# Optimization experiments

Hardware: AMD Instinct MI355X
Metric: run time of the kernel (lower is better)

## Reference

```python
import jax, jax.numpy as jnp
import numpy as np

E, DM, DH, K, DIL = 8, 512, 1024, 3, 2
N, L = 128, 128
PAD = DIL * (K - 1) // 2  # 'same' padding


def _conv1d(x, w):
    # x: [N, Cin, L], w: [Cout, Cin, K] -> [N, Cout, L]
    return jax.lax.conv_general_dilated(
        x, w, window_strides=(1,), padding=[(PAD, PAD)],
        rhs_dilation=(DIL,), dimension_numbers=("NCH", "OIH", "NCH"))


def _moe_conv(x, W, B, onehot):
    # W: [E, Cout, Cin, K], B: [E, Cout], onehot: [N, E]
    ys = jax.vmap(lambda w, b: _conv1d(x, w) + b[None, :, None])(W, B)  # [E, N, Cout, L]
    return jnp.einsum("enol,ne->nol", ys, onehot)


def setup_inputs() -> dict:
    key = jax.random.key(0)
    k1, k2, k3, k4, k5 = jax.random.split(key, 5)
    inp = jax.random.normal(k1, (N, DM, L), dtype=jnp.float32)
    # uneven per-expert sample counts summing to N (samples pre-sorted by expert)
    fwd_expert_count = jnp.asarray(np.array([10, 20, 16, 16, 12, 22, 14, 18], dtype=np.int32))
    w1 = jax.random.normal(k2, (E, DH, DM, K), dtype=jnp.float32) * 0.02
    b1 = jax.random.normal(k3, (E, DH), dtype=jnp.float32) * 0.02
    w2 = jax.random.normal(k4, (E, DM, DH, K), dtype=jnp.float32) * 0.02
    b2 = jax.random.normal(k5, (E, DM), dtype=jnp.float32) * 0.02
    return {"inp": inp, "fwd_expert_count": fwd_expert_count,
            "w1": w1, "b1": b1, "w2": w2, "b2": b2}


def reference(inp, fwd_expert_count, w1, b1, w2, b2):
    # map each sample index to its expert via cumulative counts
    cs = jnp.cumsum(fwd_expert_count)
    eid = jnp.searchsorted(cs, jnp.arange(N), side="right")  # [N]
    onehot = (eid[:, None] == jnp.arange(E)[None, :]).astype(inp.dtype)  # [N, E]
    h = _moe_conv(inp, w1, b1, onehot)       # [N, DH, L]
    h = jax.nn.gelu(h)
    out = _moe_conv(h, w2, b2, onehot)       # [N, DM, L]
    return out
```

## Files before the change

kernel.cpp:

```cpp
#include <hip/hip_runtime.h>
#include <hip/hip_bf16.h>
#include <stdint.h>


typedef __attribute__((ext_vector_type(8))) short short8;
typedef __attribute__((ext_vector_type(4))) float f32x4;

#define NSAMP 128
#define DMV 512
#define DHV 1024

#define OFF_X   0ull
#define OFF_H   (16ull << 20)
#define OFF_W1  (48ull << 20)
#define OFF_W2  (72ull << 20)

__device__ __forceinline__ uint16_t f2bf(float f) {
  uint32_t u = __builtin_bit_cast(uint32_t, f);
  uint32_t r = (u + 0x7FFFu + ((u >> 16) & 1u)) >> 16;
  return (uint16_t)r;
}

__device__ __forceinline__ void async_copy16(const void* g, void* l) {
  __builtin_amdgcn_global_load_lds(
      (const __attribute__((address_space(1))) uint32_t*)g,
      (__attribute__((address_space(3))) uint32_t*)l, 16, 0, 0);
}

__device__ __forceinline__ float gelu_f(float x) {
  float u = 0.7978845608028654f * (x + 0.044715f * x * x * x);
  float t = __expf(2.0f * u);
  float th = 1.0f - 2.0f / (t + 1.0f);
  return 0.5f * x * (1.0f + th);
}

__global__ void prep_x(const float* __restrict__ inp, uint16_t* __restrict__ xp) {
  uint32_t t = blockIdx.x * 256u + threadIdx.x;
  uint32_t sub = t & 3u;
  uint32_t l = (t >> 2) & 127u;
  uint32_t cc = (t >> 9) & 15u;
  uint32_t s = t >> 13;
  uint32_t fl = ((l + 2u) >> 1) & 3u;
  uint32_t c0 = cc * 32u + ((sub ^ fl) & 3u) * 8u;
  const float* src = inp + ((size_t)s * DMV + c0) * 128u + l;
  uint32_t pk[4];
#pragma unroll
  for (int p = 0; p < 4; ++p) {
    uint32_t lo = f2bf(src[(size_t)(2 * p) * 128u]);
    uint32_t hi = f2bf(src[(size_t)(2 * p + 1) * 128u]);
    pk[p] = lo | (hi << 16);
  }
  uint4 v; v.x = pk[0]; v.y = pk[1]; v.z = pk[2]; v.w = pk[3];
  ((uint4*)xp)[t] = v;
}

__global__ void prep_w(const float* __restrict__ w, uint16_t* __restrict__ wp,
                       int C, int mtBits, int ccBits) {
  uint32_t t = blockIdx.x * 256u + threadIdx.x;
  uint32_t sub = t & 3u;
  uint32_t row = (t >> 2) & 127u;
  uint32_t t2 = t >> 9;
  uint32_t k = t2 % 3u;
  uint32_t t3 = t2 / 3u;
  uint32_t mt = t3 & ((1u << mtBits) - 1u);
  uint32_t t4 = t3 >> mtBits;
  uint32_t cc = t4 & ((1u << ccBits) - 1u);
  uint32_t e = t4 >> ccBits;
  uint32_t O = 128u << mtBits;
  uint32_t o = mt * 128u + row;
  uint32_t c0 = cc * 32u + ((sub ^ (row >> 1)) & 3u) * 8u;
  const float* src = w + (((size_t)e * O + o) * (uint32_t)C + c0) * 3u + k;
  uint32_t pk[4];
#pragma unroll
  for (int p = 0; p < 4; ++p) {
    uint32_t lo = f2bf(src[(size_t)(2 * p) * 3u]);
    uint32_t hi = f2bf(src[(size_t)(2 * p + 1) * 3u]);
    pk[p] = lo | (hi << 16);
  }
  uint4 v; v.x = pk[0]; v.y = pk[1]; v.z = pk[2]; v.w = pk[3];
  ((uint4*)wp)[t] = v;
}

template <int PHASE>
__global__ __launch_bounds__(512, 2) void conv_mfma(
    const uint16_t* __restrict__ bprep, const uint16_t* __restrict__ wprep,
    const float* __restrict__ bias, const int* __restrict__ cnt,
    uint16_t* __restrict__ hout, float* __restrict__ fout) {
  constexpr int CC = (PHASE == 1) ? 16 : 32;
  constexpr int HALVES = (PHASE == 1) ? 2 : 1;
  constexpr int MTP = (PHASE == 1) ? 8 : 4;
  constexpr int AREP = 4 * HALVES;
  constexpr int OO = (PHASE == 1) ? DHV : DMV;
  constexpr uint32_t AS = HALVES * 24576u;
  constexpr uint32_t BUFS = AS + 16896u;

  uint32_t b = blockIdx.x;
  uint32_t work = (b & 7u) * 32u + (b >> 3);
  const int pr = work & 63;
  const int mt = work >> 6;
  int e = 0;
  {
    int cum = cnt[0];
    while (2 * pr >= cum && e < 7) { ++e; cum += cnt[e]; }
  }
  const int tid = threadIdx.x;
  const int lane = tid & 63;
  const int wv = tid >> 6;
  const int wr = wv >> 2, wc = wv & 3;
  const int l15 = lane & 15, kg = lane >> 4;

  __shared__ __align__(16) uint8_t lds[2 * BUFS];

  uint32_t aOff[AREP];
#pragma unroll
  for (int a = 0; a < AREP; ++a) {
    uint32_t R = (uint32_t)(wr * (AREP * 16) + a * 16 + l15);
    uint32_t h = R >> 7, ri = R & 127u;
    aOff[a] = h * 24576u + ri * 64u + (((uint32_t)kg ^ (ri >> 1)) & 3u) * 16u;
  }
  uint32_t lB[4];
#pragma unroll
  for (int bq = 0; bq < 4; ++bq) lB[bq] = (uint32_t)((wc & 1) * 64 + bq * 16 + l15);
  const uint32_t pOff = AS + (uint32_t)(wc >> 1) * 8448u;
  const int mtBase = (PHASE == 1) ? mt * 2 : mt;

  auto STAGE = [&](int buf, int cc) {
    uint8_t* bb = lds + (uint32_t)buf * BUFS;
    const uint16_t* wsrc = wprep + (((size_t)e * CC + cc) * MTP + mtBase) * 12288;
#pragma unroll
    for (int i = 0; i < 3 * HALVES; ++i)
      async_copy16(wsrc + i * 4096 + tid * 8, bb + (uint32_t)i * 8192u + tid * 16);
#pragma unroll
    for (int p = 0; p < 2; ++p)
      async_copy16(bprep + (((size_t)(2 * pr + p)) * CC + cc) * 4096 + tid * 8,
                   bb + AS + (uint32_t)p * 8448u + 128u + tid * 16);
  };

  if (tid < 64) {
    uint32_t n = (uint32_t)tid >> 5, rest = (uint32_t)tid & 31u;
    uint32_t p = rest >> 4, ri = (rest >> 2) & 3u, sb = rest & 3u;
    uint32_t rowByte = (ri < 2) ? ri * 64u : (8320u + (ri - 2) * 64u);
    uint4 z = make_uint4(0, 0, 0, 0);
    *(uint4*)(lds + n * BUFS + AS + p * 8448u + rowByte + sb * 16u) = z;
  }
  STAGE(0, 0);
  __syncthreads();

  f32x4 acc[AREP][4] = {};

#pragma unroll 2
  for (int cc = 0; cc < CC; ++cc) {
    int cur = cc & 1;
    if (cc + 1 < CC) STAGE(cur ^ 1, cc + 1);
    const uint8_t* bb = lds + (uint32_t)cur * BUFS;
#pragma unroll
    for (int k = 0; k < 3; ++k) {
      short8 af[AREP], bf[4];
#pragma unroll
      for (int a = 0; a < AREP; ++a)
        af[a] = *(const short8*)(bb + aOff[a] + (uint32_t)k * 8192u);
#pragma unroll
      for (int bq = 0; bq < 4; ++bq) {
        uint32_t r = lB[bq] + 2u * (uint32_t)k;
        bf[bq] = *(const short8*)(bb + pOff + r * 64u +
                                  (((uint32_t)kg ^ (r >> 1)) & 3u) * 16u);
      }
#pragma unroll
      for (int a = 0; a < AREP; ++a)
#pragma unroll
        for (int bq = 0; bq < 4; ++bq)
          acc[a][bq] = __builtin_amdgcn_mfma_f32_16x16x32_bf16(af[a], bf[bq], acc[a][bq], 0, 0, 0);
    }
    __syncthreads();
  }

  const int p = wc >> 1;
  const int s = 2 * pr + p;
  if (PHASE == 1) {
#pragma unroll
    for (int a = 0; a < AREP; ++a) {
      int ob = mt * 256 + wr * 128 + a * 16 + kg * 4;
      float4 bv = *(const float4*)(bias + (size_t)e * OO + ob);
      int cc2 = mt * 8 + wr * 4 + (a >> 1);
      uint32_t g = (uint32_t)((a & 1) * 2 + (kg >> 1));
      uint32_t j0 = (uint32_t)((kg & 1) * 4);
#pragma unroll
      for (int bq = 0; bq < 4; ++bq) {
        int l = (wc & 1) * 64 + bq * 16 + l15;
        uint32_t flq = ((uint32_t)(l + 2) >> 1) & 3u;
        uint32_t sub = g ^ flq;
        float v0 = gelu_f(acc[a][bq][0] + bv.x);
        float v1 = gelu_f(acc[a][bq][1] + bv.y);
        float v2 = gelu_f(acc[a][bq][2] + bv.z);
        float v3 = gelu_f(acc[a][bq][3] + bv.w);
        uint2 pk;
        pk.x = (uint32_t)f2bf(v0) | ((uint32_t)f2bf(v1) << 16);
        pk.y = (uint32_t)f2bf(v2) | ((uint32_t)f2bf(v3) << 16);
        size_t ci = ((size_t)s * 32 + cc2) * 128 + l;
        *(uint2*)(hout + ci * 32 + sub * 8 + j0) = pk;
      }
    }
  } else {
#pragma unroll
    for (int a = 0; a < AREP; ++a) {
      int ob = mt * 128 + wr * 64 + a * 16 + kg * 4;
      float4 bv = *(const float4*)(bias + (size_t)e * OO + ob);
      float bvr[4] = {bv.x, bv.y, bv.z, bv.w};
      float* op = fout + ((size_t)s * DMV + ob) * 128;
#pragma unroll
      for (int bq = 0; bq < 4; ++bq) {
        int l = (wc & 1) * 64 + bq * 16 + l15;
#pragma unroll
        for (int r = 0; r < 4; ++r)
          op[(size_t)r * 128 + l] = acc[a][bq][r] + bvr[r];
      }
    }
  }
}

extern "C" void kernel_launch(void* const* d_in, const int* in_sizes, int n_in,
                              void* d_out, int out_size, void* d_ws, size_t ws_size,
                              hipStream_t stream) {
  const float* inp = (const float*)d_in[0];
  const int* cnt = (const int*)d_in[1];
  const float* w1 = (const float*)d_in[2];
  const float* b1 = (const float*)d_in[3];
  const float* w2 = (const float*)d_in[4];
  const float* b2 = (const float*)d_in[5];
  float* out = (float*)d_out;
  uint8_t* ws = (uint8_t*)d_ws;
  uint16_t* xp = (uint16_t*)(ws + OFF_X);
  uint16_t* hp = (uint16_t*)(ws + OFF_H);
  uint16_t* w1p = (uint16_t*)(ws + OFF_W1);
  uint16_t* w2p = (uint16_t*)(ws + OFF_W2);

  prep_x<<<dim3(4096), dim3(256), 0, stream>>>(inp, xp);
  prep_w<<<dim3(6144), dim3(256), 0, stream>>>(w1, w1p, 512, 3, 4);
  prep_w<<<dim3(6144), dim3(256), 0, stream>>>(w2, w2p, 1024, 2, 5);
  conv_mfma<1><<<dim3(256), dim3(512), 0, stream>>>(xp, w1p, b1, cnt, hp, nullptr);
  conv_mfma<2><<<dim3(256), dim3(512), 0, stream>>>(hp, w2p, b2, cnt, nullptr, out);
}
```

Baseline: 160.8 us.

## Interleave async staging with MFMA steps and fuse prep kernels into one launch

The conv main loop is restructured into fine-grained steps. Each step issues part of the next chunk's global-to-LDS copies, then waits with explicit vmcnt counts and raw s_barrier instead of a full __syncthreads per chunk, and raises wave priority around the MFMA block. A-tile rows are remapped so each wave row group reads its own half in phase 1. The three prep kernels are merged into one launch to cut launch overhead. Hand-counted waitcnt values risk races if the copy order or counts are wrong, and the extra barriers per step add sync cost.

```diff
diff --git a/kernel.cpp b/kernel.cpp
--- a/kernel.cpp
+++ b/kernel.cpp
@@ -6,7 +6,6 @@
 typedef __attribute__((ext_vector_type(8))) short short8;
 typedef __attribute__((ext_vector_type(4))) float f32x4;
 
-#define NSAMP 128
 #define DMV 512
 #define DHV 1024
 
@@ -14,6 +13,9 @@
 #define OFF_H   (16ull << 20)
 #define OFF_W1  (48ull << 20)
 #define OFF_W2  (72ull << 20)
+
+#define VMW(n) asm volatile("s_waitcnt vmcnt(" #n ")" ::: "memory")
+#define VMNOP  do {} while (0)
 
 __device__ __forceinline__ uint16_t f2bf(float f) {
   uint32_t u = __builtin_bit_cast(uint32_t, f);
@@ -34,8 +36,8 @@
   return 0.5f * x * (1.0f + th);
 }
 
-__global__ void prep_x(const float* __restrict__ inp, uint16_t* __restrict__ xp) {
-  uint32_t t = blockIdx.x * 256u + threadIdx.x;
+__device__ __forceinline__ void prep_x_body(uint32_t t, const float* __restrict__ inp,
+                                            uint16_t* __restrict__ xp) {
   uint32_t sub = t & 3u;
   uint32_t l = (t >> 2) & 127u;
   uint32_t cc = (t >> 9) & 15u;
@@ -54,9 +56,9 @@
   ((uint4*)xp)[t] = v;
 }
 
-__global__ void prep_w(const float* __restrict__ w, uint16_t* __restrict__ wp,
-                       int C, int mtBits, int ccBits) {
-  uint32_t t = blockIdx.x * 256u + threadIdx.x;
+__device__ __forceinline__ void prep_w_body(uint32_t t, const float* __restrict__ w,
+                                            uint16_t* __restrict__ wp,
+                                            int C, int mtBits, int ccBits) {
   uint32_t sub = t & 3u;
   uint32_t row = (t >> 2) & 127u;
   uint32_t t2 = t >> 9;
@@ -81,6 +83,41 @@
   ((uint4*)wp)[t] = v;
 }
 
+__global__ void prep_all(const float* __restrict__ inp,
+                         const float* __restrict__ w1, const float* __restrict__ w2,
+                         uint16_t* __restrict__ xp,
+                         uint16_t* __restrict__ w1p, uint16_t* __restrict__ w2p) {
+  uint32_t b = blockIdx.x, tid = threadIdx.x;
+  if (b < 4096u)        prep_x_body(b * 256u + tid, inp, xp);
+  else if (b < 10240u)  prep_w_body((b - 4096u) * 256u + tid, w1, w1p, 512, 3, 4);
+  else                  prep_w_body((b - 10240u) * 256u + tid, w2, w2p, 1024, 2, 5);
+}
+
+#define PHASE_STEP(K, HH, READB, STAGE_BODY, VM_BODY)                          \
+  {                                                                            \
+    short8 af_[4];                                                             \
+    _Pragma("unroll") for (int q = 0; q < 4; ++q)                              \
+      af_[q] = *(const short8*)(br + aOff[(HH) * 4 + q] + (uint32_t)(K) * 8192u); \
+    if (READB) {                                                               \
+      _Pragma("unroll") for (int bq = 0; bq < 4; ++bq) {                       \
+        uint32_t r_ = lB[bq] + 2u * (uint32_t)(K);                             \
+        bfk[bq] = *(const short8*)(br + pOff + r_ * 64u +                      \
+                    (((uint32_t)kg ^ (r_ >> 1)) & 3u) * 16u);                  \
+      }                                                                        \
+    }                                                                          \
+    STAGE_BODY;                                                                \
+    VM_BODY;                                                                   \
+    __builtin_amdgcn_s_barrier();                                              \
+    asm volatile("s_waitcnt lgkmcnt(0)" ::: "memory");                         \
+    __builtin_amdgcn_s_setprio(1);                                             \
+    _Pragma("unroll") for (int q = 0; q < 4; ++q)                              \
+      _Pragma("unroll") for (int bq = 0; bq < 4; ++bq)                         \
+        acc[(HH) * 4 + q][bq] = __builtin_amdgcn_mfma_f32_16x16x32_bf16(       \
+            af_[q], bfk[bq], acc[(HH) * 4 + q][bq], 0, 0, 0);                  \
+    __builtin_amdgcn_s_setprio(0);                                             \
+    __builtin_amdgcn_s_barrier();                                              \
+  }
+
 template <int PHASE>
 __global__ __launch_bounds__(512, 2) void conv_mfma(
     const uint16_t* __restrict__ bprep, const uint16_t* __restrict__ wprep,
@@ -114,9 +151,10 @@
   uint32_t aOff[AREP];
 #pragma unroll
   for (int a = 0; a < AREP; ++a) {
-    uint32_t R = (uint32_t)(wr * (AREP * 16) + a * 16 + l15);
-    uint32_t h = R >> 7, ri = R & 127u;
-    aOff[a] = h * 24576u + ri * 64u + (((uint32_t)kg ^ (ri >> 1)) & 3u) * 16u;
+    uint32_t ri = (HALVES == 2) ? (uint32_t)(a * 16 + l15)
+                                : (uint32_t)(wr * 64 + a * 16 + l15);
+    uint32_t base = (HALVES == 2) ? (uint32_t)wr * 24576u : 0u;
+    aOff[a] = base + ri * 64u + (((uint32_t)kg ^ (ri >> 1)) & 3u) * 16u;
   }
   uint32_t lB[4];
 #pragma unroll
@@ -124,16 +162,14 @@
   const uint32_t pOff = AS + (uint32_t)(wc >> 1) * 8448u;
   const int mtBase = (PHASE == 1) ? mt * 2 : mt;
 
-  auto STAGE = [&](int buf, int cc) {
-    uint8_t* bb = lds + (uint32_t)buf * BUFS;
-    const uint16_t* wsrc = wprep + (((size_t)e * CC + cc) * MTP + mtBase) * 12288;
-#pragma unroll
-    for (int i = 0; i < 3 * HALVES; ++i)
-      async_copy16(wsrc + i * 4096 + tid * 8, bb + (uint32_t)i * 8192u + tid * 16);
-#pragma unroll
-    for (int p = 0; p < 2; ++p)
-      async_copy16(bprep + (((size_t)(2 * pr + p)) * CC + cc) * 4096 + tid * 8,
-                   bb + AS + (uint32_t)p * 8448u + 128u + tid * 16);
+  const uint16_t* wTile0 = wprep + ((size_t)e * CC * MTP + mtBase) * 12288;
+  auto SA = [&](uint8_t* bw, int ccn, int h, int k) {
+    async_copy16(wTile0 + (size_t)ccn * (MTP * 12288) + (h * 3 + k) * 4096 + tid * 8,
+                 bw + (uint32_t)(h * 3 + k) * 8192u + (uint32_t)tid * 16);
+  };
+  auto SBL = [&](uint8_t* bw, int ccn, int p) {
+    async_copy16(bprep + ((size_t)(2 * pr + p) * CC + ccn) * 4096 + tid * 8,
+                 bw + AS + (uint32_t)p * 8448u + 128u + (uint32_t)tid * 16);
   };
 
   if (tid < 64) {
@@ -143,35 +179,62 @@
     uint4 z = make_uint4(0, 0, 0, 0);
     *(uint4*)(lds + n * BUFS + AS + p * 8448u + rowByte + sb * 16u) = z;
   }
-  STAGE(0, 0);
-  __syncthreads();
+  asm volatile("s_waitcnt lgkmcnt(0)" ::: "memory");
+
+  if (PHASE == 1) {
+    SBL(lds, 0, 0); SBL(lds, 0, 1);
+    SA(lds, 0, 0, 0); SA(lds, 0, 1, 0);
+    SA(lds, 0, 0, 1); SA(lds, 0, 1, 1);
+    SA(lds, 0, 0, 2); SA(lds, 0, 1, 2);
+    VMW(4);
+  } else {
+    SBL(lds, 0, 0); SBL(lds, 0, 1);
+    SA(lds, 0, 0, 0); SA(lds, 0, 0, 1); SA(lds, 0, 0, 2);
+    VMW(2);
+  }
+  __builtin_amdgcn_s_barrier();
 
   f32x4 acc[AREP][4] = {};
-
-#pragma unroll 2
-  for (int cc = 0; cc < CC; ++cc) {
-    int cur = cc & 1;
-    if (cc + 1 < CC) STAGE(cur ^ 1, cc + 1);
-    const uint8_t* bb = lds + (uint32_t)cur * BUFS;
-#pragma unroll
-    for (int k = 0; k < 3; ++k) {
-      short8 af[AREP], bf[4];
-#pragma unroll
-      for (int a = 0; a < AREP; ++a)
-        af[a] = *(const short8*)(bb + aOff[a] + (uint32_t)k * 8192u);
-#pragma unroll
-      for (int bq = 0; bq < 4; ++bq) {
-        uint32_t r = lB[bq] + 2u * (uint32_t)k;
-        bf[bq] = *(const short8*)(bb + pOff + r * 64u +
-                                  (((uint32_t)kg ^ (r >> 1)) & 3u) * 16u);
-      }
-#pragma unroll
-      for (int a = 0; a < AREP; ++a)
-#pragma unroll
-        for (int bq = 0; bq < 4; ++bq)
-          acc[a][bq] = __builtin_amdgcn_mfma_f32_16x16x32_bf16(af[a], bf[bq], acc[a][bq], 0, 0, 0);
-    }
-    __syncthreads();
+  short8 bfk[4];
+
+  if (PHASE == 1) {
+#pragma unroll 1
+    for (int cc = 0; cc < CC - 1; ++cc) {
+      const uint8_t* br = lds + (uint32_t)(cc & 1) * BUFS;
+      uint8_t* bw = lds + (uint32_t)((cc & 1) ^ 1) * BUFS;
+      const int cn = cc + 1;
+      PHASE_STEP(0, 0, true,  { SBL(bw, cn, 0); SBL(bw, cn, 1); }, VMNOP);
+      PHASE_STEP(0, 1, false, { SA(bw, cn, 0, 0); SA(bw, cn, 1, 0); }, VMW(6));
+      PHASE_STEP(1, 0, true,  { SA(bw, cn, 0, 1); }, VMNOP);
+      PHASE_STEP(1, 1, false, { SA(bw, cn, 1, 1); }, VMW(6));
+      PHASE_STEP(2, 0, true,  { SA(bw, cn, 0, 2); }, VMNOP);
+      PHASE_STEP(2, 1, false, { SA(bw, cn, 1, 2); }, VMW(4));
+    }
+    {
+      const uint8_t* br = lds + (uint32_t)((CC - 1) & 1) * BUFS;
+      PHASE_STEP(0, 0, true,  {}, VMNOP);
+      PHASE_STEP(0, 1, false, {}, VMW(2));
+      PHASE_STEP(1, 0, true,  {}, VMNOP);
+      PHASE_STEP(1, 1, false, {}, VMW(0));
+      PHASE_STEP(2, 0, true,  {}, VMNOP);
+      PHASE_STEP(2, 1, false, {}, VMNOP);
+    }
+  } else {
+#pragma unroll 1
+    for (int cc = 0; cc < CC - 1; ++cc) {
+      const uint8_t* br = lds + (uint32_t)(cc & 1) * BUFS;
+      uint8_t* bw = lds + (uint32_t)((cc & 1) ^ 1) * BUFS;
+      const int cn = cc + 1;
+      PHASE_STEP(0, 0, true, { SBL(bw, cn, 0); SBL(bw, cn, 1); SA(bw, cn, 0, 0); }, VMW(4));
+      PHASE_STEP(1, 0, true, { SA(bw, cn, 0, 1); }, VMW(4));
+      PHASE_STEP(2, 0, true, { SA(bw, cn, 0, 2); }, VMW(2));
+    }
+    {
+      const uint8_t* br = lds + (uint32_t)((CC - 1) & 1) * BUFS;
+      PHASE_STEP(0, 0, true, {}, VMW(1));
+      PHASE_STEP(1, 0, true, {}, VMW(0));
+      PHASE_STEP(2, 0, true, {}, VMNOP);
+    }
   }
 
   const int p = wc >> 1;
@@ -234,9 +297,7 @@
   uint16_t* w1p = (uint16_t*)(ws + OFF_W1);
   uint16_t* w2p = (uint16_t*)(ws + OFF_W2);
 
-  prep_x<<<dim3(4096), dim3(256), 0, stream>>>(inp, xp);
-  prep_w<<<dim3(6144), dim3(256), 0, stream>>>(w1, w1p, 512, 3, 4);
-  prep_w<<<dim3(6144), dim3(256), 0, stream>>>(w2, w2p, 1024, 2, 5);
+  prep_all<<<dim3(16384), dim3(256), 0, stream>>>(inp, w1, w2, xp, w1p, w2p);
   conv_mfma<1><<<dim3(256), dim3(512), 0, stream>>>(xp, w1p, b1, cnt, hp, nullptr);
   conv_mfma<2><<<dim3(256), dim3(512), 0, stream>>>(hp, w2p, b2, cnt, nullptr, out);
 }
```

New measurement: 162.3 us. Within noise of the previous version (+0.9%).
